# Performance work log

Hardware: AMD Instinct MI355X
Metric: run time of the kernel (lower is better)

Reference implementation:

```python
import jax, jax.numpy as jnp
import numpy as np

FEAT = 1024
BATCH = 8192
GRID_SIZE = 5
SPLINE_ORDER = 3
GRID_RANGE = (-1.0, 1.0)


def make_grid(in_features):
    # efficient-kan extended grid: (in_features, grid_size + 2*spline_order + 1)
    h = (GRID_RANGE[1] - GRID_RANGE[0]) / GRID_SIZE
    g = jnp.arange(-SPLINE_ORDER, GRID_SIZE + SPLINE_ORDER + 1, dtype=jnp.float32) * h + GRID_RANGE[0]
    return jnp.broadcast_to(g, (in_features, g.shape[0]))


def b_splines(x, grid):
    # x: (B, in), grid: (in, G+2k+1) -> bases: (B, in, G+k)  (Cox-de Boor)
    x = x[..., None]
    bases = ((x >= grid[:, :-1]) & (x < grid[:, 1:])).astype(x.dtype)
    for k in range(1, SPLINE_ORDER + 1):
        left = (x - grid[:, : -(k + 1)]) / (grid[:, k:-1] - grid[:, : -(k + 1)])
        right = (grid[:, k + 1:] - x) / (grid[:, k + 1:] - grid[:, 1:-k])
        bases = left * bases[:, :, :-1] + right * bases[:, :, 1:]
    return bases


def kan_linear(x, base_w, spline_w):
    # base path: SiLU(x) @ base_w^T ; spline path: per-input-feature basis weighted sum
    grid = make_grid(x.shape[-1])
    base = jax.nn.silu(x) @ base_w.T                        # (B, out)
    sp = jnp.einsum('big,oig->bo', b_splines(x, grid), spline_w)
    return base + sp


def setup_inputs() -> dict:
    key = jax.random.key(0)
    ks = jax.random.split(key, 8)
    nb = GRID_SIZE + SPLINE_ORDER  # 8 basis functions per input feature
    return {
        'feat1': jax.random.normal(ks[0], (BATCH, FEAT), jnp.float32),
        'feat2': jax.random.normal(ks[1], (BATCH, FEAT), jnp.float32),
        'attn_w': jax.random.normal(ks[2], (FEAT, 2 * FEAT), jnp.float32) * 0.02,
        'attn_b': jnp.zeros((FEAT,), jnp.float32),
        'base_w0': jax.random.normal(ks[3], (FEAT, 2 * FEAT), jnp.float32) * 0.02,
        'spline_w0': jax.random.normal(ks[4], (FEAT, 2 * FEAT, nb), jnp.float32) * 0.02,
        'base_w1': jax.random.normal(ks[5], (FEAT, FEAT), jnp.float32) * 0.03,
        'spline_w1': jax.random.normal(ks[6], (FEAT, FEAT, nb), jnp.float32) * 0.03,
    }


def reference(feat1, feat2, attn_w, attn_b, base_w0, spline_w0, base_w1, spline_w1):
    combined = jnp.concatenate([feat1, feat2], axis=-1)          # (B, 2F)
    attention = jax.nn.sigmoid(combined @ attn_w.T + attn_b)     # (B, F)
    kan_in = jnp.concatenate([feat1 * attention, feat2 * (1.0 - attention)], axis=-1)
    h = kan_linear(kan_in, base_w0, spline_w0)                   # (B, F)
    fused = kan_linear(h, base_w1, spline_w1)                    # (B, F)
    return fused
```

## Files before the change

### kernel.cpp

```cpp
#include <hip/hip_runtime.h>
#include <hip/hip_bf16.h>
#include <stdint.h>

#define DEVINL __device__ __forceinline__

typedef unsigned short u16;
typedef unsigned int   u32;
typedef unsigned long long u64;

using short8 = __attribute__((ext_vector_type(8))) short;
using f32x4  = __attribute__((ext_vector_type(4))) float;

DEVINL u16 f2bf(float f) {
  u32 u = __builtin_bit_cast(u32, f);
  return (u16)((u + 0x7fffu + ((u >> 16) & 1u)) >> 16);
}
DEVINL float bf2f(u16 v) { return __builtin_bit_cast(float, ((u32)v) << 16); }

typedef const unsigned int __attribute__((address_space(1)))* gas1_t;
typedef unsigned int __attribute__((address_space(3)))* las3_t;

DEVINL void gl_lds16(const void* g, void* l) {
  __builtin_amdgcn_global_load_lds((gas1_t)(uintptr_t)g, (las3_t)(uintptr_t)l, 16, 0, 0);
}

__global__ void cvt_bf16_kernel(const float* __restrict__ s, u16* __restrict__ d, int n4) {
  int i = blockIdx.x * 256 + threadIdx.x;
  if (i >= n4) return;
  float4 v = ((const float4*)s)[i];
  u32 lo = (u32)f2bf(v.x) | ((u32)f2bf(v.y) << 16);
  u32 hi = (u32)f2bf(v.z) | ((u32)f2bf(v.w) << 16);
  ((uint2*)d)[i] = make_uint2(lo, hi);
}

__global__ void build_combined_kernel(const float* __restrict__ f1,
                                      const float* __restrict__ f2,
                                      u16* __restrict__ d) {
  int i = blockIdx.x * 256 + threadIdx.x;
  int row = i >> 9, c4 = i & 511;
  const float* s = (c4 < 256) ? (f1 + (size_t)row * 1024 + c4 * 4)
                              : (f2 + (size_t)row * 1024 + (c4 - 256) * 4);
  float4 v = *(const float4*)s;
  u32 lo = (u32)f2bf(v.x) | ((u32)f2bf(v.y) << 16);
  u32 hi = (u32)f2bf(v.z) | ((u32)f2bf(v.w) << 16);
  ((uint2*)d)[i] = make_uint2(lo, hi);
}

constexpr int BM = 128, BK = 64;

template <int BN, bool SPLINE, int EPI>
__global__ __launch_bounds__((BN == 256) ? 512 : 256)
void kan_gemm(const u16* __restrict__ Asrc, const u16* __restrict__ Bw,
              int K, int lda,
              const float* __restrict__ bias,
              const float* __restrict__ f1g, const float* __restrict__ f2g,
              u16* __restrict__ o_a, u16* __restrict__ o_b,
              const float* addsrc, float* outf) {
  constexpr int THREADS = (BN == 256) ? 512 : 256;
  constexpr int WN = BN / 64;
  constexpr int AR = (BM * BK) / (THREADS * 8);
  constexpr int BR = (BN * BK) / (THREADS * 8);

  __shared__ __align__(16) u16 As[BM * BK];
  __shared__ __align__(16) u16 Bs[BN * BK];

  const int tid = threadIdx.x;
  const int lane = tid & 63;
  const int wv = tid >> 6;
  const int wm = wv / WN, wn = wv % WN;
  const int l15 = lane & 15, lhi = lane >> 4;
  const int m0 = blockIdx.x * BM, n0 = blockIdx.y * BN;

  f32x4 acc[4][4] = {};

  for (int kt = 0; kt < K; kt += BK) {
    if constexpr (!SPLINE) {
#pragma unroll
      for (int r = 0; r < AR; ++r) {
        int e = (r * THREADS + tid) * 8;
        int row = e >> 6, col = e & 63;
        gl_lds16(Asrc + (size_t)(m0 + row) * lda + kt + col, &As[e]);
      }
    } else {
#pragma unroll
      for (int s = 0; s < (BM * 8) / THREADS; ++s) {
        int e = tid + s * THREADS;
        int row = e >> 3, xc = e & 7;
        float xv = bf2f(Asrc[(size_t)(m0 + row) * lda + (kt >> 3) + xc]);
        float uu = fmaf(xv, 2.5f, 5.5f);
        float fl = floorf(uu);
        int p = (int)fl;
        float t = uu - fl;
        bool valid = (uu >= 0.0f) && (uu < 11.0f);
        float t2 = t * t, t3 = t2 * t;
        float s1 = 1.0f - t;
        float v0 = t3 * (1.0f / 6.0f);
        float v1 = fmaf(t3, -0.5f, fmaf(t2, 0.5f, fmaf(t, 0.5f, 1.0f / 6.0f)));
        float v2 = fmaf(t3, 0.5f, fmaf(t2, -1.0f, 2.0f / 3.0f));
        float v3 = s1 * s1 * s1 * (1.0f / 6.0f);
        u64 wp = (u64)f2bf(v3) | ((u64)f2bf(v2) << 16) |
                 ((u64)f2bf(v1) << 32) | ((u64)f2bf(v0) << 48);
        if (!valid) wp = 0;
        int pcl = p < 0 ? 0 : (p > 10 ? 10 : p);
        int sb = (pcl << 4) - 48;
        u32 wd[4];
#pragma unroll
        for (int wi = 0; wi < 4; ++wi) {
          int dd = 32 * wi - sb;
          u32 val = 0;
          if (dd > -32 && dd < 64)
            val = (dd >= 0) ? (u32)(wp >> dd) : (u32)(wp << (-dd));
          wd[wi] = val;
        }
        *(uint4*)&As[(row << 6) + (xc << 3)] = make_uint4(wd[0], wd[1], wd[2], wd[3]);
      }
    }
#pragma unroll
    for (int r = 0; r < BR; ++r) {
      int e = (r * THREADS + tid) * 8;
      int row = e >> 6, col = e & 63;
      gl_lds16(Bw + (size_t)(n0 + row) * K + kt + col, &Bs[e]);
    }
    __syncthreads();
#pragma unroll
    for (int ks = 0; ks < BK; ks += 32) {
      short8 av[4], bv[4];
#pragma unroll
      for (int i = 0; i < 4; ++i)
        av[i] = *(const short8*)&As[(wm * 64 + i * 16 + l15) * BK + ks + lhi * 8];
#pragma unroll
      for (int j = 0; j < 4; ++j)
        bv[j] = *(const short8*)&Bs[(wn * 64 + j * 16 + l15) * BK + ks + lhi * 8];
#pragma unroll
      for (int i = 0; i < 4; ++i)
#pragma unroll
        for (int j = 0; j < 4; ++j)
          acc[i][j] = __builtin_amdgcn_mfma_f32_16x16x32_bf16(av[i], bv[j], acc[i][j], 0, 0, 0);
    }
    __syncthreads();
  }

  const int rbase = m0 + wm * 64 + lhi * 4;
  const int cbase = n0 + wn * 64 + l15;
#pragma unroll
  for (int i = 0; i < 4; ++i) {
#pragma unroll
    for (int r = 0; r < 4; ++r) {
      const int grow = rbase + i * 16 + r;
#pragma unroll
      for (int j = 0; j < 4; ++j) {
        const int gcol = cbase + j * 16;
        float v = acc[i][j][r];
        if constexpr (EPI == 0) {
          float att = 1.0f / (1.0f + __expf(-(v + bias[gcol])));
          float a1 = f1g[(size_t)grow * 1024 + gcol] * att;
          float a2 = f2g[(size_t)grow * 1024 + gcol] * (1.0f - att);
          size_t b0i = (size_t)grow * 2048 + gcol;
          o_a[b0i]        = f2bf(a1);
          o_a[b0i + 1024] = f2bf(a2);
          o_b[b0i]        = f2bf(a1 / (1.0f + __expf(-a1)));
          o_b[b0i + 1024] = f2bf(a2 / (1.0f + __expf(-a2)));
        } else if constexpr (EPI == 1) {
          outf[(size_t)grow * 1024 + gcol] = v;
        } else if constexpr (EPI == 2) {
          size_t ix = (size_t)grow * 1024 + gcol;
          float h = v + addsrc[ix];
          o_a[ix] = f2bf(h);
          o_b[ix] = f2bf(h / (1.0f + __expf(-h)));
        } else {
          size_t ix = (size_t)grow * 1024 + gcol;
          outf[ix] = v + addsrc[ix];
        }
      }
    }
  }
}

extern "C" void kernel_launch(void* const* d_in, const int* in_sizes, int n_in,
                              void* d_out, int out_size, void* d_ws, size_t ws_size,
                              hipStream_t stream) {
  const float* feat1     = (const float*)d_in[0];
  const float* feat2     = (const float*)d_in[1];
  const float* attn_w    = (const float*)d_in[2];
  const float* attn_b    = (const float*)d_in[3];
  const float* base_w0   = (const float*)d_in[4];
  const float* spline_w0 = (const float*)d_in[5];
  const float* base_w1   = (const float*)d_in[6];
  const float* spline_w1 = (const float*)d_in[7];
  float* out = (float*)d_out;
  char*  ws  = (char*)d_ws;

  u16* attn_w_bf    = (u16*)(ws + 0);
  u16* base_w0_bf   = (u16*)(ws + 4194304);
  u16* spline_w0_bf = (u16*)(ws + 8388608);
  u16* combined     = (u16*)(ws + 41943040);
  u16* h_bf         = combined;
  u16* silu1        = (u16*)(ws + 41943040 + 16777216);
  u16* x0           = (u16*)(ws + 75497472);
  u16* base_w1_bf   = x0;
  u16* spline_w1_bf = (u16*)(ws + 75497472 + 2097152);
  u16* silu0        = (u16*)(ws + 109051904);
  float* h32        = (float*)(ws + 142606336);

  auto cvt = [&](const float* s, u16* d, int n) {
    int n4 = n >> 2;
    cvt_bf16_kernel<<<(n4 + 255) / 256, 256, 0, stream>>>(s, d, n4);
  };

  cvt(attn_w, attn_w_bf, 1024 * 2048);
  cvt(base_w0, base_w0_bf, 1024 * 2048);
  cvt(spline_w0, spline_w0_bf, 1024 * 2048 * 8);
  build_combined_kernel<<<16384, 256, 0, stream>>>(feat1, feat2, combined);

  dim3 g128(8192 / 128, 1024 / 128);
  dim3 g256(8192 / 128, 1024 / 256);

  kan_gemm<128, false, 0><<<g128, 256, 0, stream>>>(
      combined, attn_w_bf, 2048, 2048, attn_b, feat1, feat2, x0, silu0, nullptr, nullptr);
  kan_gemm<128, false, 1><<<g128, 256, 0, stream>>>(
      silu0, base_w0_bf, 2048, 2048, nullptr, nullptr, nullptr, nullptr, nullptr, nullptr, h32);
  kan_gemm<256, true, 2><<<g256, 512, 0, stream>>>(
      x0, spline_w0_bf, 16384, 2048, nullptr, nullptr, nullptr, h_bf, silu1, h32, nullptr);
  cvt(base_w1, base_w1_bf, 1024 * 1024);
  cvt(spline_w1, spline_w1_bf, 1024 * 1024 * 8);
  kan_gemm<128, false, 1><<<g128, 256, 0, stream>>>(
      silu1, base_w1_bf, 1024, 1024, nullptr, nullptr, nullptr, nullptr, nullptr, nullptr, out);
  kan_gemm<256, true, 3><<<g256, 512, 0, stream>>>(
      h_bf, spline_w1_bf, 8192, 1024, nullptr, nullptr, nullptr, nullptr, nullptr, out, out);
}
```

Baseline: 1.247 ms.

## Precompute B-spline bases into workspace and run spline GEMMs as plain async-loaded GEMMs

When the workspace is large enough, a separate kernel expands each activation into 8 bf16 basis values and writes them to a 256MB buffer. The spline GEMMs then load A tiles with global_load_lds like dense GEMMs instead of computing bases inline per tile, and use BN=128 tiles. This removes the repeated basis computation, which was redone for every N-tile, and the synchronous A-path in the spline GEMM. The cost is a large extra write and read of the expanded bases through HBM. A fallback keeps the old inline path for small workspaces.

```diff
diff --git a/kernel.cpp b/kernel.cpp
--- a/kernel.cpp
+++ b/kernel.cpp
@@ -22,6 +22,35 @@
 
 DEVINL void gl_lds16(const void* g, void* l) {
   __builtin_amdgcn_global_load_lds((gas1_t)(uintptr_t)g, (las3_t)(uintptr_t)l, 16, 0, 0);
+}
+
+DEVINL uint4 bspline8(float xv) {
+  float uu = fmaf(xv, 2.5f, 5.5f);
+  float fl = floorf(uu);
+  int p = (int)fl;
+  float t = uu - fl;
+  bool valid = (uu >= 0.0f) && (uu < 11.0f);
+  float t2 = t * t, t3 = t2 * t;
+  float s1 = 1.0f - t;
+  float v0 = t3 * (1.0f / 6.0f);
+  float v1 = fmaf(t3, -0.5f, fmaf(t2, 0.5f, fmaf(t, 0.5f, 1.0f / 6.0f)));
+  float v2 = fmaf(t3, 0.5f, fmaf(t2, -1.0f, 2.0f / 3.0f));
+  float v3 = s1 * s1 * s1 * (1.0f / 6.0f);
+  u64 wp = (u64)f2bf(v3) | ((u64)f2bf(v2) << 16) |
+           ((u64)f2bf(v1) << 32) | ((u64)f2bf(v0) << 48);
+  if (!valid) wp = 0;
+  int pcl = p < 0 ? 0 : (p > 10 ? 10 : p);
+  int sb = (pcl << 4) - 48;
+  u32 wd[4];
+#pragma unroll
+  for (int wi = 0; wi < 4; ++wi) {
+    int dd = 32 * wi - sb;
+    u32 val = 0;
+    if (dd > -32 && dd < 64)
+      val = (dd >= 0) ? (u32)(wp >> dd) : (u32)(wp << (-dd));
+    wd[wi] = val;
+  }
+  return make_uint4(wd[0], wd[1], wd[2], wd[3]);
 }
 
 __global__ void cvt_bf16_kernel(const float* __restrict__ s, u16* __restrict__ d, int n4) {
@@ -44,6 +73,17 @@
   u32 lo = (u32)f2bf(v.x) | ((u32)f2bf(v.y) << 16);
   u32 hi = (u32)f2bf(v.z) | ((u32)f2bf(v.w) << 16);
   ((uint2*)d)[i] = make_uint2(lo, hi);
+}
+
+__global__ void basis_gen_kernel(const u16* __restrict__ x, u16* __restrict__ bases, int total4) {
+  for (int i = blockIdx.x * 256 + threadIdx.x; i < total4; i += gridDim.x * 256) {
+    uint2 xv = ((const uint2*)x)[i];
+    u16 xs[4] = {(u16)(xv.x & 0xffff), (u16)(xv.x >> 16),
+                 (u16)(xv.y & 0xffff), (u16)(xv.y >> 16)};
+#pragma unroll
+    for (int j = 0; j < 4; ++j)
+      ((uint4*)bases)[(size_t)i * 4 + j] = bspline8(bf2f(xs[j]));
+  }
 }
 
 constexpr int BM = 128, BK = 64;
@@ -87,32 +127,7 @@
         int e = tid + s * THREADS;
         int row = e >> 3, xc = e & 7;
         float xv = bf2f(Asrc[(size_t)(m0 + row) * lda + (kt >> 3) + xc]);
-        float uu = fmaf(xv, 2.5f, 5.5f);
-        float fl = floorf(uu);
-        int p = (int)fl;
-        float t = uu - fl;
-        bool valid = (uu >= 0.0f) && (uu < 11.0f);
-        float t2 = t * t, t3 = t2 * t;
-        float s1 = 1.0f - t;
-        float v0 = t3 * (1.0f / 6.0f);
-        float v1 = fmaf(t3, -0.5f, fmaf(t2, 0.5f, fmaf(t, 0.5f, 1.0f / 6.0f)));
-        float v2 = fmaf(t3, 0.5f, fmaf(t2, -1.0f, 2.0f / 3.0f));
-        float v3 = s1 * s1 * s1 * (1.0f / 6.0f);
-        u64 wp = (u64)f2bf(v3) | ((u64)f2bf(v2) << 16) |
-                 ((u64)f2bf(v1) << 32) | ((u64)f2bf(v0) << 48);
-        if (!valid) wp = 0;
-        int pcl = p < 0 ? 0 : (p > 10 ? 10 : p);
-        int sb = (pcl << 4) - 48;
-        u32 wd[4];
-#pragma unroll
-        for (int wi = 0; wi < 4; ++wi) {
-          int dd = 32 * wi - sb;
-          u32 val = 0;
-          if (dd > -32 && dd < 64)
-            val = (dd >= 0) ? (u32)(wp >> dd) : (u32)(wp << (-dd));
-          wd[wi] = val;
-        }
-        *(uint4*)&As[(row << 6) + (xc << 3)] = make_uint4(wd[0], wd[1], wd[2], wd[3]);
+        *(uint4*)&As[(row << 6) + (xc << 3)] = bspline8(xv);
       }
     }
 #pragma unroll
@@ -189,42 +204,78 @@
   const float* spline_w1 = (const float*)d_in[7];
   float* out = (float*)d_out;
   char*  ws  = (char*)d_ws;
-
-  u16* attn_w_bf    = (u16*)(ws + 0);
-  u16* base_w0_bf   = (u16*)(ws + 4194304);
-  u16* spline_w0_bf = (u16*)(ws + 8388608);
-  u16* combined     = (u16*)(ws + 41943040);
-  u16* h_bf         = combined;
-  u16* silu1        = (u16*)(ws + 41943040 + 16777216);
-  u16* x0           = (u16*)(ws + 75497472);
-  u16* base_w1_bf   = x0;
-  u16* spline_w1_bf = (u16*)(ws + 75497472 + 2097152);
-  u16* silu0        = (u16*)(ws + 109051904);
-  float* h32        = (float*)(ws + 142606336);
+  const size_t MB = 1048576ull;
 
   auto cvt = [&](const float* s, u16* d, int n) {
     int n4 = n >> 2;
     cvt_bf16_kernel<<<(n4 + 255) / 256, 256, 0, stream>>>(s, d, n4);
   };
 
-  cvt(attn_w, attn_w_bf, 1024 * 2048);
-  cvt(base_w0, base_w0_bf, 1024 * 2048);
-  cvt(spline_w0, spline_w0_bf, 1024 * 2048 * 8);
-  build_combined_kernel<<<16384, 256, 0, stream>>>(feat1, feat2, combined);
-
   dim3 g128(8192 / 128, 1024 / 128);
-  dim3 g256(8192 / 128, 1024 / 256);
-
-  kan_gemm<128, false, 0><<<g128, 256, 0, stream>>>(
-      combined, attn_w_bf, 2048, 2048, attn_b, feat1, feat2, x0, silu0, nullptr, nullptr);
-  kan_gemm<128, false, 1><<<g128, 256, 0, stream>>>(
-      silu0, base_w0_bf, 2048, 2048, nullptr, nullptr, nullptr, nullptr, nullptr, nullptr, h32);
-  kan_gemm<256, true, 2><<<g256, 512, 0, stream>>>(
-      x0, spline_w0_bf, 16384, 2048, nullptr, nullptr, nullptr, h_bf, silu1, h32, nullptr);
-  cvt(base_w1, base_w1_bf, 1024 * 1024);
-  cvt(spline_w1, spline_w1_bf, 1024 * 1024 * 8);
-  kan_gemm<128, false, 1><<<g128, 256, 0, stream>>>(
-      silu1, base_w1_bf, 1024, 1024, nullptr, nullptr, nullptr, nullptr, nullptr, nullptr, out);
-  kan_gemm<256, true, 3><<<g256, 512, 0, stream>>>(
-      h_bf, spline_w1_bf, 8192, 1024, nullptr, nullptr, nullptr, nullptr, nullptr, out, out);
-}
+
+  if (ws_size >= 442 * MB) {
+    u16* attn_w_bf    = (u16*)(ws + 0 * MB);
+    u16* base_w0_bf   = (u16*)(ws + 4 * MB);
+    u16* spline_w0_bf = (u16*)(ws + 8 * MB);
+    u16* base_w1_bf   = (u16*)(ws + 40 * MB);
+    u16* spline_w1_bf = (u16*)(ws + 42 * MB);
+    u16* combined     = (u16*)(ws + 58 * MB);
+    u16* h_bf         = combined;
+    u16* x0           = (u16*)(ws + 90 * MB);
+    u16* silu0        = (u16*)(ws + 122 * MB);
+    u16* silu1        = silu0;
+    float* h32        = (float*)(ws + 154 * MB);
+    u16* bases        = (u16*)(ws + 186 * MB);
+
+    cvt(attn_w, attn_w_bf, 1024 * 2048);
+    cvt(base_w0, base_w0_bf, 1024 * 2048);
+    cvt(spline_w0, spline_w0_bf, 1024 * 2048 * 8);
+    cvt(base_w1, base_w1_bf, 1024 * 1024);
+    cvt(spline_w1, spline_w1_bf, 1024 * 1024 * 8);
+    build_combined_kernel<<<16384, 256, 0, stream>>>(feat1, feat2, combined);
+
+    kan_gemm<128, false, 0><<<g128, 256, 0, stream>>>(
+        combined, attn_w_bf, 2048, 2048, attn_b, feat1, feat2, x0, silu0, nullptr, nullptr);
+    basis_gen_kernel<<<2048, 256, 0, stream>>>(x0, bases, 8192 * 2048 / 4);
+    kan_gemm<128, false, 1><<<g128, 256, 0, stream>>>(
+        silu0, base_w0_bf, 2048, 2048, nullptr, nullptr, nullptr, nullptr, nullptr, nullptr, h32);
+    kan_gemm<128, false, 2><<<g128, 256, 0, stream>>>(
+        bases, spline_w0_bf, 16384, 16384, nullptr, nullptr, nullptr, h_bf, silu1, h32, nullptr);
+    basis_gen_kernel<<<2048, 256, 0, stream>>>(h_bf, bases, 8192 * 1024 / 4);
+    kan_gemm<128, false, 1><<<g128, 256, 0, stream>>>(
+        silu1, base_w1_bf, 1024, 1024, nullptr, nullptr, nullptr, nullptr, nullptr, nullptr, out);
+    kan_gemm<128, false, 3><<<g128, 256, 0, stream>>>(
+        bases, spline_w1_bf, 8192, 8192, nullptr, nullptr, nullptr, nullptr, nullptr, out, out);
+  } else {
+    u16* attn_w_bf    = (u16*)(ws + 0);
+    u16* base_w0_bf   = (u16*)(ws + 4194304);
+    u16* spline_w0_bf = (u16*)(ws + 8388608);
+    u16* combined     = (u16*)(ws + 41943040);
+    u16* h_bf         = combined;
+    u16* silu1        = (u16*)(ws + 41943040 + 16777216);
+    u16* x0           = (u16*)(ws + 75497472);
+    u16* base_w1_bf   = x0;
+    u16* spline_w1_bf = (u16*)(ws + 75497472 + 2097152);
+    u16* silu0        = (u16*)(ws + 109051904);
+    float* h32        = (float*)(ws + 142606336);
+
+    cvt(attn_w, attn_w_bf, 1024 * 2048);
+    cvt(base_w0, base_w0_bf, 1024 * 2048);
+    cvt(spline_w0, spline_w0_bf, 1024 * 2048 * 8);
+    build_combined_kernel<<<16384, 256, 0, stream>>>(feat1, feat2, combined);
+
+    dim3 g256(8192 / 128, 1024 / 256);
+    kan_gemm<128, false, 0><<<g128, 256, 0, stream>>>(
+        combined, attn_w_bf, 2048, 2048, attn_b, feat1, feat2, x0, silu0, nullptr, nullptr);
+    kan_gemm<128, false, 1><<<g128, 256, 0, stream>>>(
+        silu0, base_w0_bf, 2048, 2048, nullptr, nullptr, nullptr, nullptr, nullptr, nullptr, h32);
+    kan_gemm<256, true, 2><<<g256, 512, 0, stream>>>(
+        x0, spline_w0_bf, 16384, 2048, nullptr, nullptr, nullptr, h_bf, silu1, h32, nullptr);
+    cvt(base_w1, base_w1_bf, 1024 * 1024);
+    cvt(spline_w1, spline_w1_bf, 1024 * 1024 * 8);
+    kan_gemm<128, false, 1><<<g128, 256, 0, stream>>>(
+        silu1, base_w1_bf, 1024, 1024, nullptr, nullptr, nullptr, nullptr, nullptr, nullptr, out);
+    kan_gemm<256, true, 3><<<g256, 512, 0, stream>>>(
+        h_bf, spline_w1_bf, 8192, 1024, nullptr, nullptr, nullptr, nullptr, nullptr, out, out);
+  }
+}
```

After: 1.245 ms. No clear change (-0.2%).
